# Optimization experiments

Measured on AMD Instinct MI355X. Metric: run time of the kernel, lower is better.

## Reference

```python
import jax, jax.numpy as jnp
import numpy as np

B, D, G, F, A = 262144, 128, 8, 80, 18  # batch, obs dim, n_games, n_features, max_actions


def setup_inputs() -> dict:
    key = jax.random.key(0)
    ks = jax.random.split(key, 10)
    s1 = 1.0 / np.sqrt(D)
    s2 = 1.0 / np.sqrt(F)
    state = jax.random.normal(ks[0], (B, D), dtype=jnp.float32)
    idx = jnp.sort(jax.random.randint(ks[1], (B,), 0, G, dtype=jnp.int32))
    W1 = jax.random.normal(ks[2], (G, F, D), dtype=jnp.float32) * s1
    b1 = jax.random.normal(ks[3], (G, F), dtype=jnp.float32) * s1
    W2 = jax.random.normal(ks[4], (F, F), dtype=jnp.float32) * s2
    b2 = jax.random.normal(ks[5], (F,), dtype=jnp.float32) * s2
    W3 = jax.random.normal(ks[6], (F, F), dtype=jnp.float32) * s2
    b3 = jax.random.normal(ks[7], (F,), dtype=jnp.float32) * s2
    W4 = jax.random.normal(ks[8], (G, A, F), dtype=jnp.float32) * s2
    b4 = jax.random.normal(ks[9], (G, A), dtype=jnp.float32) * s2
    return {"state": state, "idx": idx, "W1": W1, "b1": b1, "W2": W2, "b2": b2,
            "W3": W3, "b3": b3, "W4": W4, "b4": b4}


def reference(state, idx, W1, b1, W2, b2, W3, b3, W4, b4):
    state = state.astype(jnp.float32)
    n_games = W1.shape[0]
    # Routed first layer: each sample goes through its game's Linear(D->F).
    # Loop is over the small fixed set of games; batch dim stays vectorized.
    h1 = jnp.zeros((state.shape[0], W1.shape[1]), dtype=state.dtype)
    for g in range(n_games):
        hg = state @ W1[g].T + b1[g]  # [B, F]
        h1 = h1 + jnp.where((idx == g)[:, None], hg, jnp.zeros((), state.dtype))
    h1 = jax.nn.relu(h1)
    # Shared MLP (features == 'relu')
    h = jax.nn.relu(h1 @ W2.T + b2)
    h = jax.nn.relu(h @ W3.T + b3)
    # All per-game heads, stacked: q[b, g, a]
    q = jnp.einsum('bf,gaf->bga', h, W4) + b4  # [B, G, A]
    # Gather the head matching each sample's game (action=None branch)
    q_idx = jnp.take_along_axis(q, idx[:, None, None].astype(jnp.int32), axis=1)  # [B,1,A]
    return jnp.squeeze(q_idx, axis=1)  # [B, A]
```

## Files before the change

### kernel.cpp

```cpp
#include <hip/hip_runtime.h>


#define B_TOT   262144
#define DDIM    128
#define FDIM    80
#define ADIM    18
#define TILE    16
#define NT      16
#define SPAN_W  (TILE*NT)
#define SH      104

#define W1SW    0
#define W2SW    81920
#define W3SW    89600
#define W4SW    97280
#define WTOT    121856

typedef __attribute__((ext_vector_type(8))) short short8;
typedef __attribute__((ext_vector_type(4))) float floatx4;
typedef __attribute__((ext_vector_type(4))) int int4v;

static __device__ __forceinline__ unsigned short f2bf(float f) {
  union { float f; unsigned u; } v; v.f = f;
  unsigned r = v.u + 0x7fffu + ((v.u >> 16) & 1u);
  return (unsigned short)(r >> 16);
}

__global__ void convert_weights(const float* __restrict__ W1, const float* __restrict__ W2,
                                const float* __restrict__ W3, const float* __restrict__ W4,
                                unsigned short* __restrict__ ws) {
  int t = blockIdx.x * 256 + threadIdx.x;
  if (t >= WTOT) return;
  int chunk = t >> 9, r = t & 511;
  int lane = r >> 3, j = r & 7;
  int l16 = lane & 15, quad = lane >> 4;
  float val;
  if (chunk < 160) {
    int g = chunk / 20, rem = chunk % 20, ks = rem / 5, ct = rem % 5;
    int n = ct * 16 + l16, k = ks * 32 + quad * 8 + j;
    val = W1[(g * FDIM + n) * DDIM + k];
  } else if (chunk < 175) {
    int c = chunk - 160, ks = c / 5, ct = c % 5;
    int n = ct * 16 + l16, k = ks * 32 + quad * 8 + j;
    val = (k < FDIM) ? W2[n * FDIM + k] : 0.f;
  } else if (chunk < 190) {
    int c = chunk - 175, ks = c / 5, ct = c % 5;
    int n = ct * 16 + l16, k = ks * 32 + quad * 8 + j;
    val = (k < FDIM) ? W3[n * FDIM + k] : 0.f;
  } else {
    int c = chunk - 190, g = c / 6, rem = c % 6, ks = rem >> 1, ct = rem & 1;
    int n = ct * 16 + l16, k = ks * 32 + quad * 8 + j;
    val = (n < ADIM && k < FDIM) ? W4[(g * ADIM + n) * FDIM + k] : 0.f;
  }
  ws[t] = f2bf(val);
}

__global__ __launch_bounds__(256, 1) void gym_fused(
    const float* __restrict__ state, const int* __restrict__ idx,
    const unsigned short* __restrict__ wsw,
    const float* __restrict__ b1, const float* __restrict__ b2,
    const float* __restrict__ b3, const float* __restrict__ b4,
    float* __restrict__ out)
{
  __shared__ __align__(16) unsigned short s_h[4][TILE * SH];

  const int tid  = threadIdx.x;
  const int lane = tid & 63;
  const int wv   = tid >> 6;
  const int l16  = lane & 15;
  const int quad = lane >> 4;
  unsigned short* hbuf = s_h[wv];
  const size_t row0w = ((size_t)blockIdx.x * 4 + wv) * SPAN_W;
  const short8 zero8 = {0, 0, 0, 0, 0, 0, 0, 0};

  if (lane < 32) {
    int r = lane >> 1, cc = lane & 1;
    *(short8*)(hbuf + r * SH + 80 + cc * 8) = zero8;
  }

  short8 w2f[15], w3f[15];
#pragma unroll
  for (int i = 0; i < 15; ++i) w2f[i] = *(const short8*)(wsw + W2SW + i * 512 + lane * 8);
#pragma unroll
  for (int i = 0; i < 15; ++i) w3f[i] = *(const short8*)(wsw + W3SW + i * 512 + lane * 8);
  float b2v[5], b3v[5];
#pragma unroll
  for (int ct = 0; ct < 5; ++ct) {
    b2v[ct] = b2[ct * 16 + l16];
    b3v[ct] = b3[ct * 16 + l16];
  }

  short8 w1f[20], w4f[6];
  float b1v[5], b4v[2];
  int curr_g = idx[row0w];
#define STAGE_GAME(G)                                                              \
  do {                                                                             \
    _Pragma("unroll")                                                              \
    for (int i = 0; i < 20; ++i)                                                   \
      w1f[i] = *(const short8*)(wsw + W1SW + ((G) * 20 + i) * 512 + lane * 8);     \
    _Pragma("unroll")                                                              \
    for (int i = 0; i < 6; ++i)                                                    \
      w4f[i] = *(const short8*)(wsw + W4SW + ((G) * 6 + i) * 512 + lane * 8);      \
    _Pragma("unroll")                                                              \
    for (int ct = 0; ct < 5; ++ct) b1v[ct] = b1[(G) * FDIM + ct * 16 + l16];       \
    _Pragma("unroll")                                                              \
    for (int ct = 0; ct < 2; ++ct) {                                               \
      int col = ct * 16 + l16;                                                     \
      b4v[ct] = (col < ADIM) ? b4[(G) * ADIM + col] : 0.f;                         \
    }                                                                              \
  } while (0)
  STAGE_GAME(curr_g);

  floatx4 praw[8];
  int4v pidx;
  {
    const float* sp = state + (row0w + l16) * DDIM + quad * 8;
#pragma unroll
    for (int ks = 0; ks < 4; ++ks) {
      praw[ks * 2]     = *(const floatx4*)(sp + ks * 32);
      praw[ks * 2 + 1] = *(const floatx4*)(sp + ks * 32 + 4);
    }
    pidx = *(const int4v*)(idx + row0w + quad * 4);
  }

  for (int t = 0; t < NT; ++t) {
    const size_t trow = row0w + (size_t)t * TILE;

    short8 afrag[4];
#pragma unroll
    for (int ks = 0; ks < 4; ++ks) {
      floatx4 va = praw[ks * 2], vb = praw[ks * 2 + 1];
      short8 f;
      f[0] = (short)f2bf(va[0]); f[1] = (short)f2bf(va[1]);
      f[2] = (short)f2bf(va[2]); f[3] = (short)f2bf(va[3]);
      f[4] = (short)f2bf(vb[0]); f[5] = (short)f2bf(vb[1]);
      f[6] = (short)f2bf(vb[2]); f[7] = (short)f2bf(vb[3]);
      afrag[ks] = f;
    }
    int4v cidx = pidx;
    const int tg_lo = __shfl(cidx[0], 0);
    const int tg_hi = __shfl(cidx[3], 48);

    {
      const size_t nrow = (t + 1 < NT) ? trow + TILE : row0w;
      const float* sp = state + (nrow + l16) * DDIM + quad * 8;
#pragma unroll
      for (int ks = 0; ks < 4; ++ks) {
        praw[ks * 2]     = *(const floatx4*)(sp + ks * 32);
        praw[ks * 2 + 1] = *(const floatx4*)(sp + ks * 32 + 4);
      }
      pidx = *(const int4v*)(idx + nrow + quad * 4);
    }

    for (int g = tg_lo; g <= tg_hi; ++g) {
      if (g != curr_g) { STAGE_GAME(g); curr_g = g; }

      {
        floatx4 acc[5];
#pragma unroll
        for (int ct = 0; ct < 5; ++ct) acc[ct] = (floatx4){0.f, 0.f, 0.f, 0.f};
#pragma unroll
        for (int ks = 0; ks < 4; ++ks)
#pragma unroll
          for (int ct = 0; ct < 5; ++ct)
            acc[ct] = __builtin_amdgcn_mfma_f32_16x16x32_bf16(afrag[ks], w1f[ks * 5 + ct], acc[ct], 0, 0, 0);
#pragma unroll
        for (int ct = 0; ct < 5; ++ct) {
          int col = ct * 16 + l16;
#pragma unroll
          for (int r = 0; r < 4; ++r) {
            if (cidx[r] == g) {
              int row = quad * 4 + r;
              hbuf[row * SH + col] = f2bf(fmaxf(acc[ct][r] + b1v[ct], 0.f));
            }
          }
        }
      }
#pragma unroll
      for (int L = 0; L < 2; ++L) {
        short8 a[3];
#pragma unroll
        for (int ks = 0; ks < 3; ++ks)
          a[ks] = *(const short8*)(hbuf + l16 * SH + ks * 32 + quad * 8);
        floatx4 acc[5];
#pragma unroll
        for (int ct = 0; ct < 5; ++ct) acc[ct] = (floatx4){0.f, 0.f, 0.f, 0.f};
#pragma unroll
        for (int ks = 0; ks < 3; ++ks)
#pragma unroll
          for (int ct = 0; ct < 5; ++ct) {
            short8 bf = (L == 0) ? w2f[ks * 5 + ct] : w3f[ks * 5 + ct];
            acc[ct] = __builtin_amdgcn_mfma_f32_16x16x32_bf16(a[ks], bf, acc[ct], 0, 0, 0);
          }
#pragma unroll
        for (int ct = 0; ct < 5; ++ct) {
          int col = ct * 16 + l16;
          float bv = (L == 0) ? b2v[ct] : b3v[ct];
#pragma unroll
          for (int r = 0; r < 4; ++r) {
            int row = quad * 4 + r;
            hbuf[row * SH + col] = f2bf(fmaxf(acc[ct][r] + bv, 0.f));
          }
        }
      }
      {
        short8 a3[3];
#pragma unroll
        for (int ks = 0; ks < 3; ++ks)
          a3[ks] = *(const short8*)(hbuf + l16 * SH + ks * 32 + quad * 8);
        floatx4 acc[2];
#pragma unroll
        for (int ct = 0; ct < 2; ++ct) acc[ct] = (floatx4){0.f, 0.f, 0.f, 0.f};
#pragma unroll
        for (int ks = 0; ks < 3; ++ks)
#pragma unroll
          for (int ct = 0; ct < 2; ++ct)
            acc[ct] = __builtin_amdgcn_mfma_f32_16x16x32_bf16(a3[ks], w4f[ks * 2 + ct], acc[ct], 0, 0, 0);
#pragma unroll
        for (int ct = 0; ct < 2; ++ct) {
          int col = ct * 16 + l16;
          if (col < ADIM) {
#pragma unroll
            for (int r = 0; r < 4; ++r) {
              if (cidx[r] == g)
                out[(trow + quad * 4 + r) * ADIM + col] = acc[ct][r] + b4v[ct];
            }
          }
        }
      }
    }
  }
#undef STAGE_GAME
}

extern "C" void kernel_launch(void* const* d_in, const int* in_sizes, int n_in,
                              void* d_out, int out_size, void* d_ws, size_t ws_size,
                              hipStream_t stream) {
  const float* state = (const float*)d_in[0];
  const int*   idx   = (const int*)d_in[1];
  const float* W1    = (const float*)d_in[2];
  const float* b1    = (const float*)d_in[3];
  const float* W2    = (const float*)d_in[4];
  const float* b2    = (const float*)d_in[5];
  const float* W3    = (const float*)d_in[6];
  const float* b3    = (const float*)d_in[7];
  const float* W4    = (const float*)d_in[8];
  const float* b4    = (const float*)d_in[9];
  float*       out   = (float*)d_out;
  unsigned short* wsw = (unsigned short*)d_ws;

  convert_weights<<<(WTOT + 255) / 256, 256, 0, stream>>>(W1, W2, W3, W4, wsw);
  gym_fused<<<B_TOT / (4 * SPAN_W), 256, 0, stream>>>(state, idx, wsw, b1, b2, b3, b4, out);
}
```

Before: 249.3 us.

## Move weights to LDS, fold biases into padded K, swap MFMA operands

W1 for the current game and W2/W3 are now staged in shared memory instead of per-lane registers, and occupancy rises to 512-thread blocks with four waves per SIMD. Biases b2/b3/b4 are folded into the padded K column: a constant 1.0 is written into the hidden buffer and the bias sits in the weight row. MFMA operands are swapped so each lane holds four consecutive features for one row, which allows packed 2-element bf16 stores and vector output writes. The explicit next-tile state prefetch is dropped in favour of more resident waves hiding latency. Game switches now need block-wide syncs, and W4 is read straight from global memory on every use.

```diff
diff --git a/kernel.cpp b/kernel.cpp
--- a/kernel.cpp
+++ b/kernel.cpp
@@ -5,10 +5,11 @@
 #define DDIM    128
 #define FDIM    80
 #define ADIM    18
-#define TILE    16
-#define NT      16
-#define SPAN_W  (TILE*NT)
 #define SH      104
+#define THREADS 512
+#define SLAB    128
+#define NSLAB   4
+#define GRID    (B_TOT / (SLAB * NSLAB))
 
 #define W1SW    0
 #define W2SW    81920
@@ -16,19 +17,34 @@
 #define W4SW    97280
 #define WTOT    121856
 
+#define LW1     0
+#define LW2     10240
+#define LW3     17920
+#define LHB     25600
+#define LDS_SH  38912
+
 typedef __attribute__((ext_vector_type(8))) short short8;
+typedef __attribute__((ext_vector_type(4))) short short4v;
+typedef __attribute__((ext_vector_type(2))) unsigned int uint2v;
 typedef __attribute__((ext_vector_type(4))) float floatx4;
-typedef __attribute__((ext_vector_type(4))) int int4v;
+typedef __attribute__((ext_vector_type(2))) float floatx2;
 
 static __device__ __forceinline__ unsigned short f2bf(float f) {
   union { float f; unsigned u; } v; v.f = f;
   unsigned r = v.u + 0x7fffu + ((v.u >> 16) & 1u);
   return (unsigned short)(r >> 16);
 }
+static __device__ __forceinline__ unsigned pk2(float a, float b) {
+  union { float f; unsigned u; } x, y; x.f = a; y.f = b;
+  unsigned ra = x.u + 0x7fffu + ((x.u >> 16) & 1u);
+  unsigned rb = y.u + 0x7fffu + ((y.u >> 16) & 1u);
+  return (ra >> 16) | (rb & 0xffff0000u);
+}
 
 __global__ void convert_weights(const float* __restrict__ W1, const float* __restrict__ W2,
                                 const float* __restrict__ W3, const float* __restrict__ W4,
-                                unsigned short* __restrict__ ws) {
+                                const float* __restrict__ b2, const float* __restrict__ b3,
+                                const float* __restrict__ b4, unsigned short* __restrict__ ws) {
   int t = blockIdx.x * 256 + threadIdx.x;
   if (t >= WTOT) return;
   int chunk = t >> 9, r = t & 511;
@@ -42,118 +58,100 @@
   } else if (chunk < 175) {
     int c = chunk - 160, ks = c / 5, ct = c % 5;
     int n = ct * 16 + l16, k = ks * 32 + quad * 8 + j;
-    val = (k < FDIM) ? W2[n * FDIM + k] : 0.f;
+    val = (k < FDIM) ? W2[n * FDIM + k] : (k == FDIM ? b2[n] : 0.f);
   } else if (chunk < 190) {
     int c = chunk - 175, ks = c / 5, ct = c % 5;
     int n = ct * 16 + l16, k = ks * 32 + quad * 8 + j;
-    val = (k < FDIM) ? W3[n * FDIM + k] : 0.f;
+    val = (k < FDIM) ? W3[n * FDIM + k] : (k == FDIM ? b3[n] : 0.f);
   } else {
     int c = chunk - 190, g = c / 6, rem = c % 6, ks = rem >> 1, ct = rem & 1;
     int n = ct * 16 + l16, k = ks * 32 + quad * 8 + j;
-    val = (n < ADIM && k < FDIM) ? W4[(g * ADIM + n) * FDIM + k] : 0.f;
+    val = (n < ADIM) ? ((k < FDIM) ? W4[(g * ADIM + n) * FDIM + k]
+                                   : (k == FDIM ? b4[g * ADIM + n] : 0.f)) : 0.f;
   }
   ws[t] = f2bf(val);
 }
 
-__global__ __launch_bounds__(256, 1) void gym_fused(
+static __device__ __forceinline__ void stage_game(
+    int g, const unsigned short* __restrict__ wsw, unsigned short* smem,
+    const float* __restrict__ b1, int tid, int quad, floatx4 b1v[5])
+{
+  __syncthreads();
+  const short8* src = (const short8*)(wsw + W1SW + g * (20 * 512));
+  short8* dst = (short8*)(smem + LW1);
+#pragma unroll
+  for (int i = 0; i < 3; ++i) {
+    int t = i * THREADS + tid;
+    if (t < 1280) dst[t] = src[t];
+  }
+  __syncthreads();
+#pragma unroll
+  for (int ct = 0; ct < 5; ++ct)
+    b1v[ct] = *(const floatx4*)(b1 + g * FDIM + ct * 16 + quad * 4);
+}
+
+__global__ __launch_bounds__(THREADS, 4) void gym_fused(
     const float* __restrict__ state, const int* __restrict__ idx,
-    const unsigned short* __restrict__ wsw,
-    const float* __restrict__ b1, const float* __restrict__ b2,
-    const float* __restrict__ b3, const float* __restrict__ b4,
+    const unsigned short* __restrict__ wsw, const float* __restrict__ b1,
     float* __restrict__ out)
 {
-  __shared__ __align__(16) unsigned short s_h[4][TILE * SH];
+  __shared__ __align__(16) unsigned short smem[LDS_SH];
 
   const int tid  = threadIdx.x;
   const int lane = tid & 63;
   const int wv   = tid >> 6;
   const int l16  = lane & 15;
   const int quad = lane >> 4;
-  unsigned short* hbuf = s_h[wv];
-  const size_t row0w = ((size_t)blockIdx.x * 4 + wv) * SPAN_W;
-  const short8 zero8 = {0, 0, 0, 0, 0, 0, 0, 0};
-
-  if (lane < 32) {
-    int r = lane >> 1, cc = lane & 1;
-    *(short8*)(hbuf + r * SH + 80 + cc * 8) = zero8;
-  }
-
-  short8 w2f[15], w3f[15];
-#pragma unroll
-  for (int i = 0; i < 15; ++i) w2f[i] = *(const short8*)(wsw + W2SW + i * 512 + lane * 8);
-#pragma unroll
-  for (int i = 0; i < 15; ++i) w3f[i] = *(const short8*)(wsw + W3SW + i * 512 + lane * 8);
-  float b2v[5], b3v[5];
-#pragma unroll
-  for (int ct = 0; ct < 5; ++ct) {
-    b2v[ct] = b2[ct * 16 + l16];
-    b3v[ct] = b3[ct * 16 + l16];
-  }
-
-  short8 w1f[20], w4f[6];
-  float b1v[5], b4v[2];
-  int curr_g = idx[row0w];
-#define STAGE_GAME(G)                                                              \
-  do {                                                                             \
-    _Pragma("unroll")                                                              \
-    for (int i = 0; i < 20; ++i)                                                   \
-      w1f[i] = *(const short8*)(wsw + W1SW + ((G) * 20 + i) * 512 + lane * 8);     \
-    _Pragma("unroll")                                                              \
-    for (int i = 0; i < 6; ++i)                                                    \
-      w4f[i] = *(const short8*)(wsw + W4SW + ((G) * 6 + i) * 512 + lane * 8);      \
-    _Pragma("unroll")                                                              \
-    for (int ct = 0; ct < 5; ++ct) b1v[ct] = b1[(G) * FDIM + ct * 16 + l16];       \
-    _Pragma("unroll")                                                              \
-    for (int ct = 0; ct < 2; ++ct) {                                               \
-      int col = ct * 16 + l16;                                                     \
-      b4v[ct] = (col < ADIM) ? b4[(G) * ADIM + col] : 0.f;                         \
-    }                                                                              \
-  } while (0)
-  STAGE_GAME(curr_g);
-
-  floatx4 praw[8];
-  int4v pidx;
+  unsigned short* hbuf = smem + LHB + wv * (16 * SH);
+  const size_t blk0 = (size_t)blockIdx.x * (SLAB * NSLAB);
+
   {
-    const float* sp = state + (row0w + l16) * DDIM + quad * 8;
-#pragma unroll
-    for (int ks = 0; ks < 4; ++ks) {
-      praw[ks * 2]     = *(const floatx4*)(sp + ks * 32);
-      praw[ks * 2 + 1] = *(const floatx4*)(sp + ks * 32 + 4);
+    const short8* src = (const short8*)(wsw + W2SW);
+    short8* dst = (short8*)(smem + LW2);
+#pragma unroll
+    for (int i = 0; i < 4; ++i) {
+      int t = i * THREADS + tid;
+      if (t < 1920) dst[t] = src[t];
     }
-    pidx = *(const int4v*)(idx + row0w + quad * 4);
-  }
-
-  for (int t = 0; t < NT; ++t) {
-    const size_t trow = row0w + (size_t)t * TILE;
+  }
+  {
+    int row = lane >> 2, grp = lane & 3;
+    short4v v = {0, 0, 0, 0};
+    if (grp == 0) v[0] = (short)0x3F80;
+    *(short4v*)(hbuf + row * SH + 80 + grp * 4) = v;
+  }
+
+  int curr_g = idx[blk0];
+  floatx4 b1v[5];
+  stage_game(curr_g, wsw, smem, b1, tid, quad, b1v);
+
+  for (int it = 0; it < NSLAB; ++it) {
+    const size_t slab0 = blk0 + (size_t)it * SLAB;
+    const size_t trow  = slab0 + wv * 16;
+    const int tg_lo = idx[slab0];
+    const int tg_hi = idx[slab0 + SLAB - 1];
+    const int midx  = idx[trow + l16];
 
     short8 afrag[4];
-#pragma unroll
-    for (int ks = 0; ks < 4; ++ks) {
-      floatx4 va = praw[ks * 2], vb = praw[ks * 2 + 1];
-      short8 f;
-      f[0] = (short)f2bf(va[0]); f[1] = (short)f2bf(va[1]);
-      f[2] = (short)f2bf(va[2]); f[3] = (short)f2bf(va[3]);
-      f[4] = (short)f2bf(vb[0]); f[5] = (short)f2bf(vb[1]);
-      f[6] = (short)f2bf(vb[2]); f[7] = (short)f2bf(vb[3]);
-      afrag[ks] = f;
+    {
+      const float* sp = state + (trow + l16) * DDIM + quad * 8;
+#pragma unroll
+      for (int ks = 0; ks < 4; ++ks) {
+        floatx4 va = *(const floatx4*)(sp + ks * 32);
+        floatx4 vb = *(const floatx4*)(sp + ks * 32 + 4);
+        short8 f;
+        unsigned u0 = pk2(va[0], va[1]), u1 = pk2(va[2], va[3]);
+        unsigned u2 = pk2(vb[0], vb[1]), u3 = pk2(vb[2], vb[3]);
+        f[0] = (short)(u0 & 0xffff); f[1] = (short)(u0 >> 16);
+        f[2] = (short)(u1 & 0xffff); f[3] = (short)(u1 >> 16);
+        f[4] = (short)(u2 & 0xffff); f[5] = (short)(u2 >> 16);
+        f[6] = (short)(u3 & 0xffff); f[7] = (short)(u3 >> 16);
+        afrag[ks] = f;
+      }
     }
-    int4v cidx = pidx;
-    const int tg_lo = __shfl(cidx[0], 0);
-    const int tg_hi = __shfl(cidx[3], 48);
-
-    {
-      const size_t nrow = (t + 1 < NT) ? trow + TILE : row0w;
-      const float* sp = state + (nrow + l16) * DDIM + quad * 8;
-#pragma unroll
-      for (int ks = 0; ks < 4; ++ks) {
-        praw[ks * 2]     = *(const floatx4*)(sp + ks * 32);
-        praw[ks * 2 + 1] = *(const floatx4*)(sp + ks * 32 + 4);
-      }
-      pidx = *(const int4v*)(idx + nrow + quad * 4);
-    }
 
     for (int g = tg_lo; g <= tg_hi; ++g) {
-      if (g != curr_g) { STAGE_GAME(g); curr_g = g; }
+      if (g != curr_g) { stage_game(g, wsw, smem, b1, tid, quad, b1v); curr_g = g; }
 
       {
         floatx4 acc[5];
@@ -162,75 +160,70 @@
 #pragma unroll
         for (int ks = 0; ks < 4; ++ks)
 #pragma unroll
-          for (int ct = 0; ct < 5; ++ct)
-            acc[ct] = __builtin_amdgcn_mfma_f32_16x16x32_bf16(afrag[ks], w1f[ks * 5 + ct], acc[ct], 0, 0, 0);
+          for (int ct = 0; ct < 5; ++ct) {
+            short8 wf = *(const short8*)(smem + LW1 + (ks * 5 + ct) * 512 + lane * 8);
+            acc[ct] = __builtin_amdgcn_mfma_f32_16x16x32_bf16(wf, afrag[ks], acc[ct], 0, 0, 0);
+          }
 #pragma unroll
         for (int ct = 0; ct < 5; ++ct) {
-          int col = ct * 16 + l16;
-#pragma unroll
-          for (int r = 0; r < 4; ++r) {
-            if (cidx[r] == g) {
-              int row = quad * 4 + r;
-              hbuf[row * SH + col] = f2bf(fmaxf(acc[ct][r] + b1v[ct], 0.f));
-            }
+          floatx4 v = acc[ct] + b1v[ct];
+          uint2v u;
+          u[0] = pk2(fmaxf(v[0], 0.f), fmaxf(v[1], 0.f));
+          u[1] = pk2(fmaxf(v[2], 0.f), fmaxf(v[3], 0.f));
+          if (midx == g)
+            *(uint2v*)(hbuf + l16 * SH + ct * 16 + quad * 4) = u;
+        }
+      }
+#pragma unroll
+      for (int L = 0; L < 2; ++L) {
+        short8 hf[3];
+#pragma unroll
+        for (int ks = 0; ks < 3; ++ks)
+          hf[ks] = *(const short8*)(hbuf + l16 * SH + ks * 32 + quad * 8);
+        floatx4 acc[5];
+#pragma unroll
+        for (int ct = 0; ct < 5; ++ct) acc[ct] = (floatx4){0.f, 0.f, 0.f, 0.f};
+        const int lw = (L == 0) ? LW2 : LW3;
+#pragma unroll
+        for (int ks = 0; ks < 3; ++ks)
+#pragma unroll
+          for (int ct = 0; ct < 5; ++ct) {
+            short8 wf = *(const short8*)(smem + lw + (ks * 5 + ct) * 512 + lane * 8);
+            acc[ct] = __builtin_amdgcn_mfma_f32_16x16x32_bf16(wf, hf[ks], acc[ct], 0, 0, 0);
           }
+#pragma unroll
+        for (int ct = 0; ct < 5; ++ct) {
+          uint2v u;
+          u[0] = pk2(fmaxf(acc[ct][0], 0.f), fmaxf(acc[ct][1], 0.f));
+          u[1] = pk2(fmaxf(acc[ct][2], 0.f), fmaxf(acc[ct][3], 0.f));
+          *(uint2v*)(hbuf + l16 * SH + ct * 16 + quad * 4) = u;
         }
       }
-#pragma unroll
-      for (int L = 0; L < 2; ++L) {
-        short8 a[3];
-#pragma unroll
-        for (int ks = 0; ks < 3; ++ks)
-          a[ks] = *(const short8*)(hbuf + l16 * SH + ks * 32 + quad * 8);
-        floatx4 acc[5];
-#pragma unroll
-        for (int ct = 0; ct < 5; ++ct) acc[ct] = (floatx4){0.f, 0.f, 0.f, 0.f};
-#pragma unroll
-        for (int ks = 0; ks < 3; ++ks)
-#pragma unroll
-          for (int ct = 0; ct < 5; ++ct) {
-            short8 bf = (L == 0) ? w2f[ks * 5 + ct] : w3f[ks * 5 + ct];
-            acc[ct] = __builtin_amdgcn_mfma_f32_16x16x32_bf16(a[ks], bf, acc[ct], 0, 0, 0);
+      {
+        short8 hf[3];
+#pragma unroll
+        for (int ks = 0; ks < 3; ++ks)
+          hf[ks] = *(const short8*)(hbuf + l16 * SH + ks * 32 + quad * 8);
+        floatx4 acc[2];
+#pragma unroll
+        for (int ct = 0; ct < 2; ++ct) acc[ct] = (floatx4){0.f, 0.f, 0.f, 0.f};
+#pragma unroll
+        for (int ks = 0; ks < 3; ++ks)
+#pragma unroll
+          for (int ct = 0; ct < 2; ++ct) {
+            short8 wf = *(const short8*)(wsw + W4SW + (g * 6 + ks * 2 + ct) * 512 + lane * 8);
+            acc[ct] = __builtin_amdgcn_mfma_f32_16x16x32_bf16(wf, hf[ks], acc[ct], 0, 0, 0);
           }
-#pragma unroll
-        for (int ct = 0; ct < 5; ++ct) {
-          int col = ct * 16 + l16;
-          float bv = (L == 0) ? b2v[ct] : b3v[ct];
-#pragma unroll
-          for (int r = 0; r < 4; ++r) {
-            int row = quad * 4 + r;
-            hbuf[row * SH + col] = f2bf(fmaxf(acc[ct][r] + bv, 0.f));
-          }
+        if (midx == g) {
+          float* op = out + (trow + l16) * ADIM;
+          *(floatx2*)(op + quad * 4)     = (floatx2){acc[0][0], acc[0][1]};
+          *(floatx2*)(op + quad * 4 + 2) = (floatx2){acc[0][2], acc[0][3]};
+          if (quad == 0)
+            *(floatx2*)(op + 16) = (floatx2){acc[1][0], acc[1][1]};
         }
       }
-      {
-        short8 a3[3];
-#pragma unroll
-        for (int ks = 0; ks < 3; ++ks)
-          a3[ks] = *(const short8*)(hbuf + l16 * SH + ks * 32 + quad * 8);
-        floatx4 acc[2];
-#pragma unroll
-        for (int ct = 0; ct < 2; ++ct) acc[ct] = (floatx4){0.f, 0.f, 0.f, 0.f};
-#pragma unroll
-        for (int ks = 0; ks < 3; ++ks)
-#pragma unroll
-          for (int ct = 0; ct < 2; ++ct)
-            acc[ct] = __builtin_amdgcn_mfma_f32_16x16x32_bf16(a3[ks], w4f[ks * 2 + ct], acc[ct], 0, 0, 0);
-#pragma unroll
-        for (int ct = 0; ct < 2; ++ct) {
-          int col = ct * 16 + l16;
-          if (col < ADIM) {
-#pragma unroll
-            for (int r = 0; r < 4; ++r) {
-              if (cidx[r] == g)
-                out[(trow + quad * 4 + r) * ADIM + col] = acc[ct][r] + b4v[ct];
-            }
-          }
-        }
-      }
     }
   }
-#undef STAGE_GAME
 }
 
 extern "C" void kernel_launch(void* const* d_in, const int* in_sizes, int n_in,
@@ -249,6 +242,6 @@
   float*       out   = (float*)d_out;
   unsigned short* wsw = (unsigned short*)d_ws;
 
-  convert_weights<<<(WTOT + 255) / 256, 256, 0, stream>>>(W1, W2, W3, W4, wsw);
-  gym_fused<<<B_TOT / (4 * SPAN_W), 256, 0, stream>>>(state, idx, wsw, b1, b2, b3, b4, out);
-}
+  convert_weights<<<(WTOT + 255) / 256, 256, 0, stream>>>(W1, W2, W3, W4, b2, b3, b4, wsw);
+  gym_fused<<<GRID, THREADS, 0, stream>>>(state, idx, wsw, b1, out);
+}
```

Result: faster. 217.9 us (-12.6%).
